# Kernel optimization log

Measured on AMD Instinct MI355X. Metric: run time of the kernel, lower is better.

The kernel has to match this reference:

```python
import jax, jax.numpy as jnp
import numpy as np


def setup_inputs() -> dict:
    key = jax.random.key(0)
    k1, k2, k3, k4 = jax.random.split(key, 4)
    B, T, E, H, D = 4, 2048, 1024, 16, 64
    x = jax.random.normal(k1, (B, T, E), dtype=jnp.float32)
    # wv stored as [E, H*D] so y = x @ wv (math-equivalent to nn.Linear weight.T)
    wv = jax.random.normal(k2, (E, H * D), dtype=jnp.float32) * (1.0 / E) ** 0.5
    wr = jax.random.normal(k3, (H, E, T), dtype=jnp.float32) * (2.0 / E) ** 0.5
    wo = jax.random.normal(k4, (H * D, E), dtype=jnp.float32) * (1.0 / (H * D)) ** 0.5
    return {"x": x, "wv": wv, "wr": wr, "wo": wo}


def reference(x, wv, wr, wo):
    B, T, E = x.shape
    H = wr.shape[0]
    HD = wv.shape[1]
    D = HD // H
    # values: [B, H, T, D]
    v = (x @ wv).reshape(B, T, H, D).transpose(0, 2, 1, 3)
    # per-key scores, identical for every query row: s[b,h,k]
    s = jnp.einsum('bte,het->bht', x, wr[:, :, :T]) / jnp.sqrt(jnp.asarray(D, x.dtype))
    # causal softmax over keys k<=q with scores shared across queries reduces to
    # a prefix-softmax-weighted cumulative sum over V (exact same math, O(T)):
    # out[q] = sum_{k<=q} exp(s_k - m) v_k / sum_{k<=q} exp(s_k - m)
    m = jnp.max(s, axis=-1, keepdims=True)          # global max is a valid stable shift
    e = jnp.exp(s - m)                              # [B,H,T]
    num = jnp.cumsum(e[..., None] * v, axis=2)      # [B,H,T,D]
    den = jnp.cumsum(e, axis=2)[..., None]          # [B,H,T,1]
    out = num / den                                 # [B,H,T,D]
    out = out.transpose(0, 2, 1, 3).reshape(B, T, HD)
    return out @ wo
```

## Files before the change

kernel.cpp:

```cpp
#include <hip/hip_runtime.h>
#include <stdint.h>

typedef unsigned short u16;
typedef __attribute__((ext_vector_type(8))) short short8;
typedef __attribute__((ext_vector_type(8))) unsigned short ushort8v;
typedef __attribute__((ext_vector_type(4))) float f32x4;

#define B_  4
#define T_  2048
#define E_  1024
#define H_  16
#define D_  64
#define HD_ 1024
#define BT_ (B_*T_)
#define TC_ 64
#define NC_ (T_/TC_)
#define SG_ 32
#define SEB_ (E_/SG_)
#define SHB_ 2

__device__ __forceinline__ u16 f2b(float f) {
  uint32_t u = __float_as_uint(f);
  uint32_t r = (u + 0x7FFFu + ((u >> 16) & 1u)) >> 16;
  return (u16)r;
}
__device__ __forceinline__ float b2f(u16 u) {
  return __uint_as_float(((uint32_t)u) << 16);
}

__global__ __launch_bounds__(256) void prep_all(const float* __restrict__ x,
                                                const float* __restrict__ wv,
                                                const float* __restrict__ wo,
                                                u16* __restrict__ xb,
                                                u16* __restrict__ xTb8,
                                                u16* __restrict__ wvT,
                                                u16* __restrict__ woT) {
  __shared__ float tile[64][65];
  const int bid = blockIdx.x;
  if (bid < 2048) {
    const int b = bid >> 9, rest = bid & 511;
    const int t0 = (rest >> 4) * 64, e0 = (rest & 15) * 64;
    const int c4 = (threadIdx.x & 15) * 4;
    const int rw = threadIdx.x >> 4;
#pragma unroll
    for (int r = 0; r < 4; ++r) {
      const int row = r * 16 + rw;
      const float4 v4 = *reinterpret_cast<const float4*>(
          &x[((size_t)b * T_ + t0 + row) * E_ + e0 + c4]);
      tile[row][c4 + 0] = v4.x; tile[row][c4 + 1] = v4.y;
      tile[row][c4 + 2] = v4.z; tile[row][c4 + 3] = v4.w;
      ushort4 o;
      o.x = f2b(v4.x); o.y = f2b(v4.y); o.z = f2b(v4.z); o.w = f2b(v4.w);
      *reinterpret_cast<ushort4*>(&xb[((size_t)(b * T_ + t0 + row)) * E_ + e0 + c4]) = o;
    }
    __syncthreads();
    const int tl = threadIdx.x & 63;
    const int eg = threadIdx.x >> 6;
#pragma unroll
    for (int p = 0; p < 2; ++p) {
      const int egg = eg + p * 4;
      ushort8v o;
#pragma unroll
      for (int j = 0; j < 8; ++j) o[j] = f2b(tile[tl][egg * 8 + j]);
      *reinterpret_cast<ushort8v*>(
          &xTb8[((size_t)(b * (E_ / 8) + (e0 >> 3) + egg) * T_ + t0 + tl) * 8]) = o;
    }
  } else {
    const int k = bid - 2048;
    const float* in = (k >> 8) ? wo : wv;
    u16* out = (k >> 8) ? woT : wvT;
    const int r0 = ((k >> 4) & 15) * 64, c0 = (k & 15) * 64;
    const int tx = threadIdx.x & 63, ty = threadIdx.x >> 6;
#pragma unroll
    for (int r = 0; r < 16; ++r) {
      int row = r * 4 + ty;
      tile[row][tx] = in[(size_t)(r0 + row) * 1024 + c0 + tx];
    }
    __syncthreads();
#pragma unroll
    for (int r = 0; r < 16; ++r) {
      int row = r * 4 + ty;
      out[(size_t)(c0 + row) * 1024 + r0 + tx] = f2b(tile[tx][row]);
    }
  }
}

template <int OUT_BF16>
__global__ __launch_bounds__(256) void gemm_bt(const u16* __restrict__ A,
                                               const u16* __restrict__ Bt,
                                               float* __restrict__ Cf,
                                               u16* __restrict__ Cb,
                                               int M, int N, int K) {
  __shared__ __align__(16) u16 As[128 * 64];
  __shared__ __align__(16) u16 Bs[128 * 64];
  const int tid  = threadIdx.x;
  const int lane = tid & 63;
  const int wave = tid >> 6;
  const int wr_  = wave >> 1, wc_ = wave & 1;

  const int nwg = gridDim.x * gridDim.y;
  const int bid = blockIdx.y * gridDim.x + blockIdx.x;
  const int cpx = nwg >> 3;
  const int swz = (bid & 7) * cpx + (bid >> 3);
  const int bx = swz % gridDim.x, by = swz / gridDim.x;
  const int brow = by * 128;
  const int bcol = bx * 128;
  const int l15 = lane & 15, l4 = lane >> 4;

  f32x4 acc[4][4];
  const f32x4 zero = {0.f, 0.f, 0.f, 0.f};
#pragma unroll
  for (int i = 0; i < 4; ++i)
#pragma unroll
    for (int j = 0; j < 4; ++j) acc[i][j] = zero;

  for (int k0 = 0; k0 < K; k0 += 64) {
#pragma unroll
    for (int s2 = 0; s2 < 4; ++s2) {
      const int c = s2 * 256 + tid;
      const int row = c >> 3, g = c & 7;
      const u16* ga = A  + (size_t)(brow + row) * K + k0 + g * 8;
      const u16* gb = Bt + (size_t)(bcol + row) * K + k0 + g * 8;
      u16* la = &As[(size_t)(s2 * 256 + wave * 64) * 8];
      u16* lb = &Bs[(size_t)(s2 * 256 + wave * 64) * 8];
      __builtin_amdgcn_global_load_lds((const __attribute__((address_space(1))) void*)ga,
                                       (__attribute__((address_space(3))) void*)la,
                                       16, 0, 0);
      __builtin_amdgcn_global_load_lds((const __attribute__((address_space(1))) void*)gb,
                                       (__attribute__((address_space(3))) void*)lb,
                                       16, 0, 0);
    }
    __syncthreads();

    short8 af[2][4], bfr[2][4];
#pragma unroll
    for (int kk = 0; kk < 2; ++kk) {
#pragma unroll
      for (int mi = 0; mi < 4; ++mi)
        af[kk][mi] = *reinterpret_cast<const short8*>(
            &As[(wr_ * 64 + mi * 16 + l15) * 64 + kk * 32 + l4 * 8]);
#pragma unroll
      for (int ni = 0; ni < 4; ++ni)
        bfr[kk][ni] = *reinterpret_cast<const short8*>(
            &Bs[(wc_ * 64 + ni * 16 + l15) * 64 + kk * 32 + l4 * 8]);
    }
#pragma unroll
    for (int kk = 0; kk < 2; ++kk)
#pragma unroll
      for (int mi = 0; mi < 4; ++mi)
#pragma unroll
        for (int ni = 0; ni < 4; ++ni)
          acc[mi][ni] = __builtin_amdgcn_mfma_f32_16x16x32_bf16(af[kk][mi], bfr[kk][ni],
                                                                acc[mi][ni], 0, 0, 0);
    __syncthreads();
  }

#pragma unroll
  for (int mi = 0; mi < 4; ++mi) {
#pragma unroll
    for (int ni = 0; ni < 4; ++ni) {
      const int col = bcol + wc_ * 64 + ni * 16 + l15;
#pragma unroll
      for (int j = 0; j < 4; ++j) {
        const int row = brow + wr_ * 64 + mi * 16 + l4 * 4 + j;
        if (OUT_BF16) Cb[(size_t)row * N + col] = f2b(acc[mi][ni][j]);
        else          Cf[(size_t)row * N + col] = acc[mi][ni][j];
      }
    }
  }
}

__global__ __launch_bounds__(256) void score_partial(const u16* __restrict__ xTb8,
                                                     const float* __restrict__ wr,
                                                     u16* __restrict__ partial) {
  const int t  = blockIdx.x * 256 + threadIdx.x;
  const int g  = blockIdx.y;
  const int h0 = blockIdx.z * SHB_;
  float acc[4][SHB_];
#pragma unroll
  for (int b = 0; b < 4; ++b)
#pragma unroll
    for (int hh = 0; hh < SHB_; ++hh) acc[b][hh] = 0.f;

#pragma unroll
  for (int e8 = 0; e8 < SEB_ / 8; ++e8) {
    const int eb = g * (SEB_ / 8) + e8;
    ushort8v xv[4];
#pragma unroll
    for (int b = 0; b < 4; ++b)
      xv[b] = *reinterpret_cast<const ushort8v*>(
          &xTb8[((size_t)(b * (E_ / 8) + eb) * T_ + t) * 8]);
#pragma unroll
    for (int j = 0; j < 8; ++j) {
      const int e = eb * 8 + j;
      float xf[4];
#pragma unroll
      for (int b = 0; b < 4; ++b) xf[b] = b2f(xv[b][j]);
#pragma unroll
      for (int hh = 0; hh < SHB_; ++hh) {
        const float w = wr[((size_t)(h0 + hh) * E_ + e) * T_ + t];
#pragma unroll
        for (int b = 0; b < 4; ++b) acc[b][hh] = fmaf(xf[b], w, acc[b][hh]);
      }
    }
  }
  u16* pp = partial + (size_t)g * (B_ * H_ * T_);
#pragma unroll
  for (int b = 0; b < 4; ++b)
#pragma unroll
    for (int hh = 0; hh < SHB_; ++hh)
      pp[((size_t)b * H_ + h0 + hh) * T_ + t] = f2b(acc[b][hh] * 0.125f);
}

__global__ __launch_bounds__(256) void chunk_sums(const u16* __restrict__ partial,
                                                  const u16* __restrict__ v,
                                                  float* __restrict__ s,
                                                  float* __restrict__ sev,
                                                  float* __restrict__ se,
                                                  float* __restrict__ mc) {
  const int bh = blockIdx.y;
  const int b = bh >> 4, h = bh & 15;
  const int w = threadIdx.x >> 6, d = threadIdx.x & 63;
  const int c = blockIdx.x * 4 + w;
  const int t = blockIdx.x * 256 + threadIdx.x;

  float sv = 0.f;
#pragma unroll
  for (int g = 0; g < SG_; ++g)
    sv += b2f(partial[(size_t)g * (B_ * H_ * T_) + (size_t)bh * T_ + t]);
  s[(size_t)bh * T_ + t] = sv;

  __shared__ float es[4][64];
  es[w][d] = sv;

  float lm = sv;
#pragma unroll
  for (int off = 1; off < 64; off <<= 1) lm = fmaxf(lm, __shfl_xor(lm, off, 64));

  const u16* vp = v + ((size_t)(b * T_ + c * TC_)) * HD_ + h * D_ + d;
  float acc = 0.f, ae = 0.f;
#pragma unroll 8
  for (int tt = 0; tt < TC_; ++tt) {
    float e = __expf(es[w][tt] - lm);
    acc = fmaf(e, b2f(vp[(size_t)tt * HD_]), acc);
    ae += e;
  }
  sev[((size_t)bh * NC_ + c) * D_ + d] = acc;
  if (d == 0) { se[bh * NC_ + c] = ae; mc[bh * NC_ + c] = lm; }
}

__global__ __launch_bounds__(256) void chunk_scan(const float* __restrict__ s,
                                                  const u16* __restrict__ v,
                                                  const float* __restrict__ sev,
                                                  const float* __restrict__ se,
                                                  const float* __restrict__ mc,
                                                  u16* __restrict__ attn) {
  const int bh = blockIdx.y;
  const int b = bh >> 4, h = bh & 15;
  const int w = threadIdx.x >> 6, d = threadIdx.x & 63;
  const int c = blockIdx.x * 4 + w;
  const float* mcp = mc + bh * NC_;

  float gm = (d < NC_) ? mcp[d] : -1e30f;
#pragma unroll
  for (int off = 1; off < 64; off <<= 1) gm = fmaxf(gm, __shfl_xor(gm, off, 64));

  const float* sevp = sev + (size_t)bh * NC_ * D_;
  const float* sep  = se + bh * NC_;
  float pn = 0.f, pd = 0.f;
  for (int c2 = 0; c2 < c; ++c2) {
    float f = __expf(mcp[c2] - gm);
    pn = fmaf(sevp[(size_t)c2 * D_ + d], f, pn);
    pd = fmaf(sep[c2], f, pd);
  }

  const float* sp = s + (size_t)bh * T_ + c * TC_;
  const u16* vp = v + ((size_t)(b * T_ + c * TC_)) * HD_ + h * D_ + d;
  u16* ap = attn + ((size_t)(b * T_ + c * TC_)) * HD_ + h * D_ + d;
#pragma unroll 8
  for (int tt = 0; tt < TC_; ++tt) {
    float e = __expf(sp[tt] - gm);
    pn = fmaf(e, b2f(vp[(size_t)tt * HD_]), pn);
    pd += e;
    ap[(size_t)tt * HD_] = f2b(__fdividef(pn, pd));
  }
}

extern "C" void kernel_launch(void* const* d_in, const int* in_sizes, int n_in,
                              void* d_out, int out_size, void* d_ws, size_t ws_size,
                              hipStream_t stream) {
  const float* x  = (const float*)d_in[0];
  const float* wv = (const float*)d_in[1];
  const float* wr = (const float*)d_in[2];
  const float* wo = (const float*)d_in[3];
  float* out = (float*)d_out;

  char* ws = (char*)d_ws;
  size_t off = 0;
  auto alloc = [&](size_t bytes) {
    void* p = ws + off;
    off += (bytes + 255) & ~(size_t)255;
    return p;
  };
  u16*   xb   = (u16*)  alloc((size_t)BT_ * E_ * 2);
  u16*   xTb8 = (u16*)  alloc((size_t)B_ * E_ * T_ * 2);
  u16*   wvT  = (u16*)  alloc((size_t)HD_ * E_ * 2);
  u16*   woT  = (u16*)  alloc((size_t)E_ * HD_ * 2);
  u16*   vv   = (u16*)  alloc((size_t)BT_ * HD_ * 2);
  u16*   attn = (u16*)  alloc((size_t)BT_ * HD_ * 2);
  float* s    = (float*)alloc((size_t)B_ * H_ * T_ * 4);
  float* sev  = (float*)alloc((size_t)B_ * H_ * NC_ * D_ * 4);
  float* se   = (float*)alloc((size_t)B_ * H_ * NC_ * 4);
  float* mc   = (float*)alloc((size_t)B_ * H_ * NC_ * 4);
  u16*   part = (u16*)  alloc((size_t)SG_ * B_ * H_ * T_ * 2);

  prep_all<<<2560, 256, 0, stream>>>(x, wv, wo, xb, xTb8, wvT, woT);

  gemm_bt<1><<<dim3(HD_ / 128, BT_ / 128), 256, 0, stream>>>(xb, wvT, nullptr, vv, BT_, HD_, E_);

  score_partial<<<dim3(T_ / 256, SG_, H_ / SHB_), 256, 0, stream>>>(xTb8, wr, part);

  chunk_sums<<<dim3(NC_ / 4, B_ * H_), 256, 0, stream>>>(part, vv, s, sev, se, mc);
  chunk_scan<<<dim3(NC_ / 4, B_ * H_), 256, 0, stream>>>(s, vv, sev, se, mc, attn);

  gemm_bt<0><<<dim3(E_ / 128, BT_ / 128), 256, 0, stream>>>(attn, woT, out, nullptr, BT_, E_, HD_);
}
```

Measured before the change: 130.3 us.

## Fuse value GEMM and score partial kernels into one interleaved launch

Merges the value-projection GEMM (512 tiles) and the score_partial kernel (2048 blocks) into a single 2560-block launch, interleaving one GEMM block for every four score blocks. The goal is to run the compute-bound MFMA GEMM alongside the memory-bound streaming of the score weights, and to remove one launch and its tail. GEMM dimensions are now hardcoded, and every block reserves the GEMM's shared memory, which may lower occupancy for the score blocks.

```diff
diff --git a/kernel.cpp b/kernel.cpp
--- a/kernel.cpp
+++ b/kernel.cpp
@@ -86,23 +86,22 @@
 }
 
 template <int OUT_BF16>
-__global__ __launch_bounds__(256) void gemm_bt(const u16* __restrict__ A,
-                                               const u16* __restrict__ Bt,
-                                               float* __restrict__ Cf,
-                                               u16* __restrict__ Cb,
-                                               int M, int N, int K) {
-  __shared__ __align__(16) u16 As[128 * 64];
-  __shared__ __align__(16) u16 Bs[128 * 64];
+__device__ __forceinline__ void gemm_body(const int vbid,
+                                          const u16* __restrict__ A,
+                                          const u16* __restrict__ Bt,
+                                          float* __restrict__ Cf,
+                                          u16* __restrict__ Cb,
+                                          u16* As, u16* Bs) {
+  const int M = BT_, N = 1024, K = 1024;
+  (void)M;
   const int tid  = threadIdx.x;
   const int lane = tid & 63;
   const int wave = tid >> 6;
   const int wr_  = wave >> 1, wc_ = wave & 1;
 
-  const int nwg = gridDim.x * gridDim.y;
-  const int bid = blockIdx.y * gridDim.x + blockIdx.x;
-  const int cpx = nwg >> 3;
-  const int swz = (bid & 7) * cpx + (bid >> 3);
-  const int bx = swz % gridDim.x, by = swz / gridDim.x;
+  const int cpx = 512 >> 3;
+  const int swz = (vbid & 7) * cpx + (vbid >> 3);
+  const int bx = swz & 7, by = swz >> 3;
   const int brow = by * 128;
   const int bcol = bx * 128;
   const int l15 = lane & 15, l4 = lane >> 4;
@@ -170,12 +169,12 @@
   }
 }
 
-__global__ __launch_bounds__(256) void score_partial(const u16* __restrict__ xTb8,
-                                                     const float* __restrict__ wr,
-                                                     u16* __restrict__ partial) {
-  const int t  = blockIdx.x * 256 + threadIdx.x;
-  const int g  = blockIdx.y;
-  const int h0 = blockIdx.z * SHB_;
+__device__ __forceinline__ void score_body(const int tx, const int g, const int hz,
+                                           const u16* __restrict__ xTb8,
+                                           const float* __restrict__ wr,
+                                           u16* __restrict__ partial) {
+  const int t  = tx * 256 + threadIdx.x;
+  const int h0 = hz * SHB_;
   float acc[4][SHB_];
 #pragma unroll
   for (int b = 0; b < 4; ++b)
@@ -210,6 +209,36 @@
 #pragma unroll
     for (int hh = 0; hh < SHB_; ++hh)
       pp[((size_t)b * H_ + h0 + hh) * T_ + t] = f2b(acc[b][hh] * 0.125f);
+}
+
+__global__ __launch_bounds__(256) void gemm1_score(const u16* __restrict__ xb,
+                                                   const u16* __restrict__ wvT,
+                                                   u16* __restrict__ vv,
+                                                   const u16* __restrict__ xTb8,
+                                                   const float* __restrict__ wr,
+                                                   u16* __restrict__ partial) {
+  __shared__ __align__(16) u16 As[128 * 64];
+  __shared__ __align__(16) u16 Bs[128 * 64];
+  const int bid = blockIdx.x;
+  const int q = bid / 5;
+  if (bid - q * 5 == 0) {
+    gemm_body<1>(q, xb, wvT, nullptr, vv, As, Bs);
+  } else {
+    const int sb = bid - q - 1;
+    const int tx = sb & 7;
+    const int g  = (sb >> 3) & 31;
+    const int hz = sb >> 8;
+    score_body(tx, g, hz, xTb8, wr, partial);
+  }
+}
+
+__global__ __launch_bounds__(256) void gemm_out(const u16* __restrict__ A,
+                                                const u16* __restrict__ Bt,
+                                                float* __restrict__ Cf) {
+  __shared__ __align__(16) u16 As[128 * 64];
+  __shared__ __align__(16) u16 Bs[128 * 64];
+  const int vbid = blockIdx.y * gridDim.x + blockIdx.x;
+  gemm_body<0>(vbid, A, Bt, Cf, nullptr, As, Bs);
 }
 
 __global__ __launch_bounds__(256) void chunk_sums(const u16* __restrict__ partial,
@@ -316,12 +345,10 @@
 
   prep_all<<<2560, 256, 0, stream>>>(x, wv, wo, xb, xTb8, wvT, woT);
 
-  gemm_bt<1><<<dim3(HD_ / 128, BT_ / 128), 256, 0, stream>>>(xb, wvT, nullptr, vv, BT_, HD_, E_);
-
-  score_partial<<<dim3(T_ / 256, SG_, H_ / SHB_), 256, 0, stream>>>(xTb8, wr, part);
+  gemm1_score<<<2560, 256, 0, stream>>>(xb, wvT, vv, xTb8, wr, part);
 
   chunk_sums<<<dim3(NC_ / 4, B_ * H_), 256, 0, stream>>>(part, vv, s, sev, se, mc);
   chunk_scan<<<dim3(NC_ / 4, B_ * H_), 256, 0, stream>>>(s, vv, sev, se, mc, attn);
 
-  gemm_bt<0><<<dim3(E_ / 128, BT_ / 128), 256, 0, stream>>>(attn, woT, out, nullptr, BT_, E_, HD_);
-}
+  gemm_out<<<dim3(HD_ / 128, BT_ / 128), 256, 0, stream>>>(attn, woT, out);
+}
```

New measurement: 145.5 us. 1.12x slower.
